# Kernel tuning notes

Hardware: AMD Instinct MI355X
Metric: run time of the kernel (lower is better)

The kernel has to match this reference:

```python
import jax, jax.numpy as jnp
import numpy as np

# --- spike logic gates on {0,1} floats (differentiable arithmetic forms) ---
def _AND(a, b): return a * b
def _OR(a, b): return a + b - a * b
def _XOR(a, b): return a + b - 2.0 * a * b
def _NOT(a): return 1.0 - a
def _MUX(s, a, b): return s * a + (1.0 - s) * b  # s==1 -> a
def _or_tree(x): return 1.0 - jnp.prod(1.0 - x, axis=-1, keepdims=True)
def _and_tree(x): return jnp.prod(x, axis=-1, keepdims=True)
def _flip(x): return x[..., ::-1]

def _cmp(a, b):
    """MSB-first bitwise comparator. Returns (a_gt_b, a_eq_b), each [...,1]."""
    eq = _NOT(_XOR(a, b))
    pre = jnp.cumprod(eq, axis=-1)                      # equal prefix incl. i
    pre_x = jnp.concatenate([jnp.ones_like(pre[..., :1]), pre[..., :-1]], -1)
    gt = jnp.sum(pre_x * a * (1.0 - b), axis=-1, keepdims=True)  # one-hot sum == OR
    return gt, pre[..., -1:]

def _add_lsb(a, b):
    """Ripple-carry adder, LSB-first. Returns (sum_bits, carry_out)."""
    c = jnp.zeros_like(a[..., :1]); outs = []
    for i in range(a.shape[-1]):
        ai = a[..., i:i+1]; bi = b[..., i:i+1]
        x = _XOR(ai, bi)
        outs.append(_XOR(x, c))
        c = _OR(ai * bi, c * x)
    return jnp.concatenate(outs, -1), c

def _sub_lsb(a, b):
    """Ripple-borrow subtractor a-b, LSB-first. Returns (diff_bits, borrow_out)."""
    br = jnp.zeros_like(a[..., :1]); outs = []
    for i in range(a.shape[-1]):
        ai = a[..., i:i+1]; bi = b[..., i:i+1]
        x = _XOR(ai, bi)
        outs.append(_XOR(x, br))
        br = _OR((1.0 - ai) * bi, br * (1.0 - x))
    return jnp.concatenate(outs, -1), br

def _bsr_sticky(m, sh5):
    """Barrel right shift of MSB-first 28-bit m by 5-bit MSB-first amount; sticky=OR of shifted-out bits."""
    st = jnp.zeros_like(m[..., :1])
    for k in range(5):
        sh = 1 << (4 - k); sb = sh5[..., k:k+1]
        shifted = jnp.concatenate([jnp.zeros_like(m[..., :sh]), m[..., :-sh]], -1)
        st = _OR(st, sb * _or_tree(m[..., -sh:]))
        m = _MUX(sb, shifted, m)
    return m, st

def _bsl(m, sh5):
    """Barrel left shift of MSB-first 28-bit m by 5-bit MSB-first amount."""
    for k in range(5):
        sh = 1 << (4 - k); sb = sh5[..., k:k+1]
        shifted = jnp.concatenate([m[..., sh:], jnp.zeros_like(m[..., :sh])], -1)
        m = _MUX(sb, shifted, m)
    return m

def _lzd28(m):
    """Leading-zero count of MSB-first 28-bit m as 5-bit MSB-first binary (28 if all zero)."""
    zc = jnp.cumprod(1.0 - m, axis=-1)
    zcx = jnp.concatenate([jnp.ones_like(zc[..., :1]), zc[..., :-1]], -1)
    oh = zcx * m                     # one-hot of first 1
    az = zc[..., -1:]                # all-zero flag
    idx = np.arange(28)
    bits = []
    for k in range(5):
        mask = jnp.asarray((idx >> (4 - k)) & 1, dtype=m.dtype)
        bits.append(jnp.sum(oh * mask, axis=-1, keepdims=True) + az * float((28 >> (4 - k)) & 1))
    return jnp.concatenate(bits, -1)

def _fp32_add(A, B):
    zeros = jnp.zeros(A.shape[:-1] + (1,), A.dtype)
    ones = jnp.ones_like(zeros)
    s_a, e_a, m_a_raw = A[..., 0:1], A[..., 1:9], A[..., 9:32]
    s_b, e_b, m_b_raw = B[..., 0:1], B[..., 1:9], B[..., 9:32]
    e_a_nonzero = _or_tree(e_a); e_a_is_zero = _NOT(e_a_nonzero); hidden_a = e_a_nonzero
    e_b_nonzero = _or_tree(e_b); e_b_is_zero = _NOT(e_b_nonzero); hidden_b = e_b_nonzero
    e_one = jnp.concatenate([zeros] * 7 + [ones], -1)
    e_a_eff = _MUX(e_a_is_zero, e_one, e_a)
    e_b_eff = _MUX(e_b_is_zero, e_one, e_b)
    m_a = jnp.concatenate([hidden_a, m_a_raw, zeros, zeros, zeros, zeros], -1)  # 28 bits
    m_b = jnp.concatenate([hidden_b, m_b_raw, zeros, zeros, zeros, zeros], -1)
    a_exp_gt, a_exp_eq = _cmp(e_a_eff, e_b_eff)
    a_mant_gt, a_mant_eq = _cmp(jnp.concatenate([hidden_a, m_a_raw], -1),
                                jnp.concatenate([hidden_b, m_b_raw], -1))
    a_abs_eq_b = _AND(a_exp_eq, a_mant_eq)
    a_mant_ge = _OR(a_mant_gt, a_mant_eq)
    a_ge_b = _OR(a_exp_gt, _AND(a_exp_eq, a_mant_ge))
    diff_ab_lsb, _ = _sub_lsb(_flip(e_a_eff), _flip(e_b_eff))
    diff_ba_lsb, _ = _sub_lsb(_flip(e_b_eff), _flip(e_a_eff))
    exp_diff = _MUX(a_ge_b, _flip(diff_ab_lsb), _flip(diff_ba_lsb))
    high_any = _or_tree(exp_diff[..., 0:3])
    bit4_and_bit3 = _AND(exp_diff[..., 3:4], exp_diff[..., 4:5])
    is_big_diff = _OR(high_any, bit4_and_bit3)
    shift_amt = exp_diff[..., 3:8]
    e_max = _MUX(a_ge_b, e_a_eff, e_b_eff)
    m_large = _MUX(a_ge_b, m_a, m_b)
    m_small_uns = _MUX(a_ge_b, m_b, m_a)
    m_small, shift_sticky = _bsr_sticky(m_small_uns, shift_amt)
    is_diff_sign = _XOR(s_a, s_b)
    exact_cancel = _AND(is_diff_sign, a_abs_eq_b)
    s_large = _MUX(a_ge_b, s_a, s_b)
    m_large_lsb = _flip(m_large); m_small_lsb = _flip(m_small)
    sum_lsb, sum_carry = _add_lsb(m_large_lsb, m_small_lsb)
    diff_lsb, _ = _sub_lsb(m_large_lsb, m_small_lsb)
    sum_result = _flip(sum_lsb); diff_result = _flip(diff_lsb)
    need_sub_one = _AND(is_diff_sign, shift_sticky)
    one_28 = jnp.concatenate([ones] + [zeros] * 27, -1)  # LSB-first 1
    diff_m1_lsb, _ = _sub_lsb(diff_lsb, one_28)
    diff_final = _MUX(need_sub_one, _flip(diff_m1_lsb), diff_result)
    mantissa_result = _MUX(is_diff_sign, diff_final, sum_result)
    result_carry = _MUX(is_diff_sign, zeros, sum_carry)
    lzc = _lzd28(mantissa_result)
    lzc_8 = jnp.concatenate([zeros, zeros, zeros, lzc], -1)
    lzc_gt, lzc_eq = _cmp(lzc_8, e_max)
    is_underflow = _OR(lzc_gt, lzc_eq)
    norm_mantissa = _bsl(mantissa_result, lzc)
    e_after_norm = _flip(_sub_lsb(_flip(e_max), _flip(lzc_8))[0])
    one_8 = jnp.concatenate([zeros] * 7 + [ones], -1)
    e_plus_one = _flip(_add_lsb(_flip(e_max), _flip(one_8))[0])
    zero_8 = jnp.concatenate([zeros] * 8, -1)
    e_normal = _MUX(is_underflow, zero_8, e_after_norm)
    final_e_pre = _MUX(result_carry, e_plus_one, e_normal)
    m_overflow = mantissa_result[..., 0:23]
    round_overflow = mantissa_result[..., 23:24]
    sticky_overflow = _or_tree(mantissa_result[..., 24:28])
    m_norm = norm_mantissa[..., 1:24]
    round_norm = norm_mantissa[..., 24:25]
    sticky_norm = _or_tree(norm_mantissa[..., 25:28])
    m_subnorm = mantissa_result[..., 0:23]
    m_pre = _MUX(result_carry, m_overflow, m_norm)
    round_pre = _MUX(result_carry, round_overflow, round_norm)
    sticky_pre_raw = _MUX(result_carry, sticky_overflow, sticky_norm)
    add_shift_sticky = _AND(_NOT(is_diff_sign), shift_sticky)
    sticky_pre = _OR(sticky_pre_raw, add_shift_sticky)
    m_selected = _MUX(is_underflow, m_subnorm, m_pre)
    L = m_selected[..., 22:23]
    do_round = _AND(_AND(round_pre, _OR(sticky_pre, L)), _NOT(is_underflow))
    m_sel_lsb = _flip(m_selected)
    m24_lsb = jnp.concatenate([m_sel_lsb, zeros], -1)
    round_inc = jnp.concatenate([do_round] + [zeros] * 23, -1)
    m_rounded_lsb, round_carry = _add_lsb(m24_lsb, round_inc)
    m_rounded = _flip(m_rounded_lsb[..., :23])
    m_final = _AND(_NOT(round_carry), m_rounded)
    exp_round_inc = jnp.concatenate([zeros] * 7 + [round_carry], -1)
    e_rounded = _flip(_add_lsb(_flip(final_e_pre), _flip(exp_round_inc))[0])
    computed_e = _MUX(round_carry, e_rounded, final_e_pre)
    computed_s = s_large
    zero_23 = jnp.zeros(A.shape[:-1] + (23,), A.dtype)
    cancel_s = _MUX(exact_cancel, zeros, computed_s)
    cancel_e = _MUX(exact_cancel, zero_8, computed_e)
    cancel_m = _MUX(exact_cancel, zero_23, m_final)
    computed_e_all_one = _and_tree(computed_e)
    ones_8 = jnp.ones_like(zero_8)
    final_s = _MUX(computed_e_all_one, computed_s, cancel_s)
    final_e = _MUX(computed_e_all_one, ones_8, cancel_e)
    final_m = _MUX(computed_e_all_one, zero_23, cancel_m)
    larger_input = _MUX(a_ge_b, A, B)
    normal_result = jnp.concatenate([final_s, final_e, final_m], -1)
    return _MUX(is_big_diff, larger_input, normal_result)

def setup_inputs() -> dict:
    key = jax.random.key(0)
    k1, k2 = jax.random.split(key)
    N = 524288
    A = jax.random.randint(k1, (N, 32), 0, 2).astype(jnp.float32)
    B = jax.random.randint(k2, (N, 32), 0, 2).astype(jnp.float32)
    return {"A": A, "B": B}

def reference(A, B):
    return _fp32_add(A, B)
```

## Files before the change

kernel.cpp:

```cpp
#include <hip/hip_runtime.h>
#include <stdint.h>

__device__ __forceinline__ uint32_t fp32_add_circuit(uint32_t a, uint32_t b) {
    const uint32_t s_a = a >> 31, s_b = b >> 31;
    const uint32_t e_a = (a >> 23) & 0xFFu, e_b = (b >> 23) & 0xFFu;
    const uint32_t hid_a = (e_a != 0u) ? 1u : 0u;
    const uint32_t hid_b = (e_b != 0u) ? 1u : 0u;
    const uint32_t e_a_eff = hid_a ? e_a : 1u;
    const uint32_t e_b_eff = hid_b ? e_b : 1u;
    const uint32_t mant_a = (hid_a << 23) | (a & 0x7FFFFFu);
    const uint32_t mant_b = (hid_b << 23) | (b & 0x7FFFFFu);

    const bool a_abs_eq_b = (e_a_eff == e_b_eff) && (mant_a == mant_b);
    const bool a_ge_b = (e_a_eff > e_b_eff) ||
                        ((e_a_eff == e_b_eff) && (mant_a >= mant_b));

    const uint32_t exp_diff = a_ge_b ? (e_a_eff - e_b_eff) : (e_b_eff - e_a_eff);
    const bool is_big_diff = exp_diff >= 24u;
    const uint32_t sh = exp_diff & 31u;

    const uint32_t e_max = a_ge_b ? e_a_eff : e_b_eff;
    const uint32_t m_large     = (a_ge_b ? mant_a : mant_b) << 4;
    const uint32_t m_small_uns = (a_ge_b ? mant_b : mant_a) << 4;
    const uint32_t m_small = m_small_uns >> sh;
    const bool shift_sticky = (m_small_uns & ((1u << sh) - 1u)) != 0u;

    const bool is_diff_sign = (s_a != s_b);
    const bool exact_cancel = is_diff_sign && a_abs_eq_b;
    const uint32_t s_large = a_ge_b ? s_a : s_b;

    const uint32_t sum = m_large + m_small;
    const uint32_t sum_carry = sum >> 28;
    const uint32_t diff0 = m_large - m_small;
    const uint32_t diff1 = (is_diff_sign && shift_sticky) ? (diff0 - 1u) : diff0;

    const uint32_t mant_res = (is_diff_sign ? diff1 : sum) & 0x0FFFFFFFu;
    const uint32_t carry = is_diff_sign ? 0u : sum_carry;

    const uint32_t lzc = mant_res ? ((uint32_t)__clz((int)mant_res) - 4u) : 28u;
    const bool is_underflow = (lzc >= e_max);
    const uint32_t norm = (mant_res << lzc) & 0x0FFFFFFFu;

    const uint32_t e_normal = is_underflow ? 0u : ((e_max - lzc) & 0xFFu);
    const uint32_t final_e_pre = carry ? ((e_max + 1u) & 0xFFu) : e_normal;

    const uint32_t m_pre     = carry ? ((mant_res >> 5) & 0x7FFFFFu)
                                     : ((norm >> 4) & 0x7FFFFFu);
    const uint32_t round_pre = carry ? ((mant_res >> 4) & 1u)
                                     : ((norm >> 3) & 1u);
    const bool sticky_raw    = carry ? ((mant_res & 0xFu) != 0u)
                                     : ((norm & 0x7u) != 0u);
    const bool sticky_pre = sticky_raw || ((!is_diff_sign) && shift_sticky);

    const uint32_t m_selected = is_underflow ? ((mant_res >> 5) & 0x7FFFFFu) : m_pre;
    const bool do_round = (round_pre != 0u) && (sticky_pre || (m_selected & 1u))
                          && !is_underflow;
    const uint32_t m24 = m_selected + (do_round ? 1u : 0u);
    const uint32_t round_carry = m24 >> 23;
    const uint32_t m_final = round_carry ? 0u : (m24 & 0x7FFFFFu);
    const uint32_t computed_e = (final_e_pre + round_carry) & 0xFFu;

    const uint32_t cs = exact_cancel ? 0u : s_large;
    const uint32_t ce = exact_cancel ? 0u : computed_e;
    const uint32_t cm = exact_cancel ? 0u : m_final;
    const bool e_all_one = (computed_e == 0xFFu);
    const uint32_t final_s = e_all_one ? s_large : cs;
    const uint32_t final_e = e_all_one ? 0xFFu : ce;
    const uint32_t final_m = e_all_one ? 0u : cm;

    const uint32_t normal_result = (final_s << 31) | (final_e << 23) | final_m;
    return is_big_diff ? (a_ge_b ? a : b) : normal_result;
}

__global__ __launch_bounds__(256)
void SpikeFP32Adder_kernel(const uint4* __restrict__ A,
                           const uint4* __restrict__ B,
                           uint4* __restrict__ O, int nrows)
{
    const int r = blockIdx.x * 256 + threadIdx.x;
    if (r >= nrows) return;
    const uint4* pa = A + (size_t)r * 8;
    const uint4* pb = B + (size_t)r * 8;

    uint32_t ua = 0u, ub = 0u;
#pragma unroll
    for (int k = 0; k < 8; ++k) {
        const uint4 va = pa[k], vb = pb[k];
        ua = (ua << 4) | (((va.x >> 23) & 1u) << 3) | (((va.y >> 23) & 1u) << 2)
                       | (((va.z >> 23) & 1u) << 1) | ((va.w >> 23) & 1u);
        ub = (ub << 4) | (((vb.x >> 23) & 1u) << 3) | (((vb.y >> 23) & 1u) << 2)
                       | (((vb.z >> 23) & 1u) << 1) | ((vb.w >> 23) & 1u);
    }

    const uint32_t res = fp32_add_circuit(ua, ub);

    uint4* po = O + (size_t)r * 8;
#pragma unroll
    for (int k = 0; k < 8; ++k) {
        uint4 vo;
        vo.x = ((res >> (31 - 4 * k)) & 1u) * 0x3F800000u;
        vo.y = ((res >> (30 - 4 * k)) & 1u) * 0x3F800000u;
        vo.z = ((res >> (29 - 4 * k)) & 1u) * 0x3F800000u;
        vo.w = ((res >> (28 - 4 * k)) & 1u) * 0x3F800000u;
        po[k] = vo;
    }
}

extern "C" void kernel_launch(void* const* d_in, const int* in_sizes, int n_in,
                              void* d_out, int out_size, void* d_ws, size_t ws_size,
                              hipStream_t stream) {
    const uint4* A = (const uint4*)d_in[0];
    const uint4* B = (const uint4*)d_in[1];
    uint4* O = (uint4*)d_out;
    const int nrows = in_sizes[0] / 32;
    const int block = 256;
    const int grid = (nrows + block - 1) / block;
    SpikeFP32Adder_kernel<<<grid, block, 0, stream>>>(A, B, O, nrows);
}
```

Baseline: 182.8 us.

## Split each row across 8 lanes with coalesced uint4 loads and shuffle packing

Each thread now loads one uint4 from each input instead of eight strided uint4s per row. The 32 bits of a row are assembled across 8 adjacent lanes using xor shuffles, every lane evaluates the adder circuit redundantly, and each lane writes its own uint4 of output. This is meant to make global loads and stores fully coalesced and to raise the number of active threads. The cost is 8x redundant scalar compute plus shuffle instructions.

```diff
diff --git a/kernel.cpp b/kernel.cpp
--- a/kernel.cpp
+++ b/kernel.cpp
@@ -1,5 +1,6 @@
 #include <hip/hip_runtime.h>
 #include <stdint.h>
+
 
 __device__ __forceinline__ uint32_t fp32_add_circuit(uint32_t a, uint32_t b) {
     const uint32_t s_a = a >> 31, s_b = b >> 31;
@@ -75,35 +76,36 @@
 __global__ __launch_bounds__(256)
 void SpikeFP32Adder_kernel(const uint4* __restrict__ A,
                            const uint4* __restrict__ B,
-                           uint4* __restrict__ O, int nrows)
+                           uint4* __restrict__ O, int nvec4)
 {
-    const int r = blockIdx.x * 256 + threadIdx.x;
-    if (r >= nrows) return;
-    const uint4* pa = A + (size_t)r * 8;
-    const uint4* pb = B + (size_t)r * 8;
+    const int gid = blockIdx.x * 256 + threadIdx.x;
+    if (gid >= nvec4) return;
+    const int m = threadIdx.x & 7;
+    const int pos = 28 - 4 * m;
 
-    uint32_t ua = 0u, ub = 0u;
-#pragma unroll
-    for (int k = 0; k < 8; ++k) {
-        const uint4 va = pa[k], vb = pb[k];
-        ua = (ua << 4) | (((va.x >> 23) & 1u) << 3) | (((va.y >> 23) & 1u) << 2)
-                       | (((va.z >> 23) & 1u) << 1) | ((va.w >> 23) & 1u);
-        ub = (ub << 4) | (((vb.x >> 23) & 1u) << 3) | (((vb.y >> 23) & 1u) << 2)
-                       | (((vb.z >> 23) & 1u) << 1) | ((vb.w >> 23) & 1u);
-    }
+    const uint4 va = A[gid];
+    const uint4 vb = B[gid];
 
-    const uint32_t res = fp32_add_circuit(ua, ub);
+    uint32_t pa = ((((va.x >> 23) & 1u) << 3) | (((va.y >> 23) & 1u) << 2) |
+                   (((va.z >> 23) & 1u) << 1) |  ((va.w >> 23) & 1u)) << pos;
+    uint32_t pb = ((((vb.x >> 23) & 1u) << 3) | (((vb.y >> 23) & 1u) << 2) |
+                   (((vb.z >> 23) & 1u) << 1) |  ((vb.w >> 23) & 1u)) << pos;
 
-    uint4* po = O + (size_t)r * 8;
-#pragma unroll
-    for (int k = 0; k < 8; ++k) {
-        uint4 vo;
-        vo.x = ((res >> (31 - 4 * k)) & 1u) * 0x3F800000u;
-        vo.y = ((res >> (30 - 4 * k)) & 1u) * 0x3F800000u;
-        vo.z = ((res >> (29 - 4 * k)) & 1u) * 0x3F800000u;
-        vo.w = ((res >> (28 - 4 * k)) & 1u) * 0x3F800000u;
-        po[k] = vo;
-    }
+    pa |= (uint32_t)__shfl_xor((int)pa, 1, 64);
+    pb |= (uint32_t)__shfl_xor((int)pb, 1, 64);
+    pa |= (uint32_t)__shfl_xor((int)pa, 2, 64);
+    pb |= (uint32_t)__shfl_xor((int)pb, 2, 64);
+    pa |= (uint32_t)__shfl_xor((int)pa, 4, 64);
+    pb |= (uint32_t)__shfl_xor((int)pb, 4, 64);
+
+    const uint32_t res = fp32_add_circuit(pa, pb);
+
+    uint4 vo;
+    vo.x = ((res >> (pos + 3)) & 1u) * 0x3F800000u;
+    vo.y = ((res >> (pos + 2)) & 1u) * 0x3F800000u;
+    vo.z = ((res >> (pos + 1)) & 1u) * 0x3F800000u;
+    vo.w = ((res >>  pos     ) & 1u) * 0x3F800000u;
+    O[gid] = vo;
 }
 
 extern "C" void kernel_launch(void* const* d_in, const int* in_sizes, int n_in,
@@ -112,8 +114,8 @@
     const uint4* A = (const uint4*)d_in[0];
     const uint4* B = (const uint4*)d_in[1];
     uint4* O = (uint4*)d_out;
-    const int nrows = in_sizes[0] / 32;
+    const int nvec4 = in_sizes[0] / 4;
     const int block = 256;
-    const int grid = (nrows + block - 1) / block;
-    SpikeFP32Adder_kernel<<<grid, block, 0, stream>>>(A, B, O, nrows);
+    const int grid = (nvec4 + block - 1) / block;
+    SpikeFP32Adder_kernel<<<grid, block, 0, stream>>>(A, B, O, nvec4);
 }
```

New measurement: 165.1 us. -9.6%, faster.
